# Performance work log

Measured on AMD Instinct MI355X. Metric: run time of the kernel, lower is better.

Reference implementation:

```python
import jax, jax.numpy as jnp
import numpy as np

B, S, H = 2, 2048, 768
NH, HD = 12, 64
I = 1152
EPS = 1e-5
ROPE_BASE = 10000.0
MAX_POS = 8192


def _layernorm(x, w, b):
    mu = jnp.mean(x, axis=-1, keepdims=True)
    var = jnp.mean(jnp.square(x - mu), axis=-1, keepdims=True)
    return (x - mu) / jnp.sqrt(var + EPS) * w + b


def _rope_tables():
    pos = jnp.arange(MAX_POS, dtype=jnp.float32)
    theta = 1.0 / (ROPE_BASE ** (jnp.arange(0, HD, 2, dtype=jnp.float32) / HD))
    ang = pos[:, None] * theta  # [MAX_POS, HD//2]
    return jnp.cos(ang), jnp.sin(ang)


def _apply_rope(x, cos, sin):
    # x: [B, NH, S, HD]; cos/sin: [B, 1, S, HD//2]; interleaved pair rotation
    x2 = x.reshape(*x.shape[:-1], HD // 2, 2)
    x0, x1 = x2[..., 0], x2[..., 1]
    rot = jnp.stack([x0 * cos - x1 * sin, x1 * cos + x0 * sin], axis=-1)
    return rot.reshape(x.shape)


def setup_inputs() -> dict:
    key = jax.random.key(0)
    ks = jax.random.split(key, 8)
    std = 0.02
    return {
        "hidden_states": jax.random.normal(ks[0], (B, S, H), dtype=jnp.float32),
        "attention_mask": jnp.zeros((B, 1, S, S), dtype=jnp.float32),
        "sliding_window_mask": jnp.zeros((B, 1, S, S), dtype=jnp.float32),
        "position_ids": jnp.tile(jnp.arange(S, dtype=jnp.int32)[None, :], (B, 1)),
        "qkv_w": jax.random.normal(ks[1], (3 * H, H), dtype=jnp.float32) * std,
        "o_w": jax.random.normal(ks[2], (H, H), dtype=jnp.float32) * std,
        "attn_norm_w": jnp.ones((H,), dtype=jnp.float32),
        "attn_norm_b": jnp.zeros((H,), dtype=jnp.float32),
        "mlp_norm_w": jnp.ones((H,), dtype=jnp.float32),
        "mlp_norm_b": jnp.zeros((H,), dtype=jnp.float32),
        "wi_w": jax.random.normal(ks[3], (2 * I, H), dtype=jnp.float32) * std,
        "wi_b": jnp.zeros((2 * I,), dtype=jnp.float32),
        "wo_w": jax.random.normal(ks[4], (H, I), dtype=jnp.float32) * std,
        "wo_b": jnp.zeros((H,), dtype=jnp.float32),
    }


def reference(hidden_states, attention_mask, sliding_window_mask, position_ids,
              qkv_w, o_w, attn_norm_w, attn_norm_b, mlp_norm_w, mlp_norm_b,
              wi_w, wi_b, wo_w, wo_b):
    # --- attention block (layer_id != 0 -> pre-LN) ---
    x = _layernorm(hidden_states, attn_norm_w, attn_norm_b)
    qkv = jnp.einsum('bsh,oh->bso', x, qkv_w)          # [B,S,3H] (no bias)
    qkv = qkv.reshape(B, S, 3, NH, HD)
    qkv = jnp.transpose(qkv, (0, 3, 2, 1, 4))          # [B,NH,3,S,HD]
    q, k, v = qkv[:, :, 0], qkv[:, :, 1], qkv[:, :, 2]

    cos_t, sin_t = _rope_tables()
    cos = cos_t[position_ids][:, None]                 # [B,1,S,HD//2]
    sin = sin_t[position_ids][:, None]
    q = _apply_rope(q, cos, sin)
    k = _apply_rope(k, cos, sin)

    scale = HD ** -0.5
    scores = jnp.einsum('bhqd,bhkd->bhqk', q, k) * scale
    scores = scores + attention_mask + sliding_window_mask
    probs = jax.nn.softmax(scores, axis=-1)
    ctx = jnp.einsum('bhqk,bhkd->bhqd', probs, v)      # [B,NH,S,HD]
    ctx = jnp.transpose(ctx, (0, 2, 1, 3)).reshape(B, S, H)
    attn_out = jnp.einsum('bsh,oh->bso', ctx, o_w)
    hidden = hidden_states + attn_out

    # --- GeGLU MLP block ---
    y = _layernorm(hidden, mlp_norm_w, mlp_norm_b)
    h = jax.nn.gelu(jnp.einsum('bsh,oh->bso', y, wi_w) + wi_b, approximate=False)
    gated = h[..., 0::2] * h[..., 1::2]                # strided gelu-gate split
    mlp_out = jnp.einsum('bsi,oi->bso', gated, wo_w) + wo_b
    return hidden + mlp_out
```

## Files before the change

### kernel.cpp

```cpp
#include <hip/hip_runtime.h>
#include <hip/hip_bf16.h>
#include <math.h>

#define B_  2
#define S_  2048
#define H_  768
#define NH_ 12
#define HD_ 64
#define I_  1152
#define LOG2E 1.4426950408889634f
#define SCALE_L2E 0.18033688011112042f

typedef __bf16 bf16;
typedef __bf16 bf16x8 __attribute__((ext_vector_type(8)));
typedef float  f32x4  __attribute__((ext_vector_type(4)));
typedef float  f32x16 __attribute__((ext_vector_type(16)));
typedef float  f32x2  __attribute__((ext_vector_type(2)));
typedef unsigned u32x2 __attribute__((ext_vector_type(2)));
typedef unsigned u32x4 __attribute__((ext_vector_type(4)));

__device__ __forceinline__ void gll16(const void* g, void* l) {
  __builtin_amdgcn_global_load_lds((const __attribute__((address_space(1))) void*)g,
                                   (__attribute__((address_space(3))) void*)l, 16, 0, 0);
}

__device__ __forceinline__ unsigned pack_bf16(float a, float b) {
  union { bf16 e[2]; unsigned u; } r;
  r.e[0] = (bf16)a; r.e[1] = (bf16)b;
  return r.u;
}

__device__ __forceinline__ void plswap(unsigned &a, unsigned &b) {
  asm volatile("v_permlane32_swap_b32 %0, %1" : "+v"(a), "+v"(b));
}
__device__ __forceinline__ float halfmax(float x) {
  unsigned a = __builtin_bit_cast(unsigned, x), b = a;
  plswap(a, b);
  return fmaxf(__builtin_bit_cast(float, a), __builtin_bit_cast(float, b));
}
__device__ __forceinline__ float halfsum(float x) {
  unsigned a = __builtin_bit_cast(unsigned, x), b = a;
  plswap(a, b);
  return __builtin_bit_cast(float, a) + __builtin_bit_cast(float, b);
}

__global__ void cvt_f32_bf16(const float* __restrict__ in, bf16* __restrict__ out, int n4) {
  int i = blockIdx.x * 256 + threadIdx.x;
  if (i >= n4) return;
  float4 v = ((const float4*)in)[i];
  union { bf16 e[4]; uint2 u; } r;
  r.e[0] = (bf16)v.x; r.e[1] = (bf16)v.y; r.e[2] = (bf16)v.z; r.e[3] = (bf16)v.w;
  ((uint2*)out)[i] = r.u;
}

__global__ void build_rope_tbl(f32x2* __restrict__ tbl) {
  int i = blockIdx.x * 256 + threadIdx.x;
  int jp = i & 31, pos = i >> 5;
  float th = exp2f((float)jp * (-13.287712379549449f / 32.f));
  float sn, cs;
  sincosf((float)pos * th, &sn, &cs);
  tbl[i] = (f32x2){cs, sn};
}

__global__ __launch_bounds__(256) void combine_mask2(const float* __restrict__ a,
                                                     const float* __restrict__ b,
                                                     bf16* __restrict__ E,
                                                     unsigned* __restrict__ flags) {
  const int kt = blockIdx.x, qi = blockIdx.y, bb = blockIdx.z, tid = threadIdx.x;
  float sm[8][4];
  bool ok = true;
#pragma unroll
  for (int c = 0; c < 8; ++c) {
    int idx4 = c * 256 + tid;
    int r = idx4 >> 4, col = (idx4 & 15) * 4;
    size_t g = ((size_t)(bb * S_) + qi * 128 + r) * S_ + kt * 64 + col;
    float4 x = *(const float4*)(a + g);
    float4 y = *(const float4*)(b + g);
    sm[c][0] = x.x + y.x; sm[c][1] = x.y + y.y;
    sm[c][2] = x.z + y.z; sm[c][3] = x.w + y.w;
    ok = ok && (sm[c][0] == 0.f) && (sm[c][1] == 0.f) && (sm[c][2] == 0.f) && (sm[c][3] == 0.f);
  }
  __shared__ unsigned sh[4];
  unsigned long long bal = __ballot(ok);
  if ((tid & 63) == 0) sh[tid >> 6] = (bal == ~0ull) ? 1u : 0u;
  __syncthreads();
  unsigned flag = sh[0] & sh[1] & sh[2] & sh[3];
  if (tid == 0) flags[(bb * 16 + qi) * 32 + kt] = flag;
  if (!flag) {
#pragma unroll
    for (int c = 0; c < 8; ++c) {
      int idx4 = c * 256 + tid;
      int r = idx4 >> 4, col = (idx4 & 15) * 4;
      size_t g = ((size_t)(bb * S_) + qi * 128 + r) * S_ + kt * 64 + col;
      union { bf16 e[4]; uint2 u; } w;
      w.e[0] = (bf16)__expf(sm[c][0]); w.e[1] = (bf16)__expf(sm[c][1]);
      w.e[2] = (bf16)__expf(sm[c][2]); w.e[3] = (bf16)__expf(sm[c][3]);
      *(uint2*)(E + g) = w.u;
    }
  }
}

__global__ __launch_bounds__(256) void ln_bf16(const float* __restrict__ in,
                                               const float* __restrict__ w,
                                               const float* __restrict__ bia,
                                               bf16* __restrict__ out) {
  int row = blockIdx.x, tid = threadIdx.x;
  const float* x = in + (size_t)row * H_;
  float v0 = x[tid], v1 = x[tid + 256], v2 = x[tid + 512];
  float s = v0 + v1 + v2;
  float q = v0 * v0 + v1 * v1 + v2 * v2;
  for (int o = 1; o < 64; o <<= 1) { s += __shfl_xor(s, o); q += __shfl_xor(q, o); }
  __shared__ float rs[4], rq[4];
  if ((tid & 63) == 0) { rs[tid >> 6] = s; rq[tid >> 6] = q; }
  __syncthreads();
  s = rs[0] + rs[1] + rs[2] + rs[3];
  q = rq[0] + rq[1] + rq[2] + rq[3];
  float mu = s * (1.f / H_);
  float var = q * (1.f / H_) - mu * mu;
  float rstd = rsqrtf(var + 1e-5f);
  bf16* orow = out + (size_t)row * H_;
  orow[tid]       = (bf16)((v0 - mu) * rstd * w[tid]       + bia[tid]);
  orow[tid + 256] = (bf16)((v1 - mu) * rstd * w[tid + 256] + bia[tid + 256]);
  orow[tid + 512] = (bf16)((v2 - mu) * rstd * w[tid + 512] + bia[tid + 512]);
}

__device__ __forceinline__ void gemm_main_loop(
    int K, const bf16* __restrict__ aSrc0, const bf16* __restrict__ aSrc1,
    const bf16* __restrict__ bSrc0, const bf16* __restrict__ bSrc1,
    bf16* As, bf16* Bs, int tid, int wr, int wc, int l15, int lg,
    f32x4 (&acc)[4][4]) {
  const int NT = K >> 5;
  auto stage = [&](int t, int buf) {
    const int ko = t * 32;
    bf16* ad = As + buf * 4096 + tid * 8;
    bf16* bd = Bs + buf * 4096 + tid * 8;
    gll16(aSrc0 + ko, ad);
    gll16(aSrc1 + ko, ad + 2048);
    gll16(bSrc0 + ko, bd);
    gll16(bSrc1 + ko, bd + 2048);
  };
  stage(0, 0);
  __syncthreads();
  for (int t = 0; t < NT; ++t) {
    const int cur = t & 1;
    if (t + 1 < NT) stage(t + 1, cur ^ 1);
    const bf16* Ab = As + cur * 4096;
    const bf16* Bb = Bs + cur * 4096;
    bf16x8 af[4], bfr[4];
#pragma unroll
    for (int i = 0; i < 4; ++i)
      af[i] = *(const bf16x8*)&Ab[(wr + i * 16 + l15) * 32 + lg * 8];
#pragma unroll
    for (int j = 0; j < 4; ++j)
      bfr[j] = *(const bf16x8*)&Bb[(wc + j * 16 + l15) * 32 + lg * 8];
    __builtin_amdgcn_s_setprio(1);
#pragma unroll
    for (int i = 0; i < 4; ++i)
#pragma unroll
      for (int j = 0; j < 4; ++j)
        acc[i][j] = __builtin_amdgcn_mfma_f32_16x16x32_bf16(af[i], bfr[j], acc[i][j], 0, 0, 0);
    __builtin_amdgcn_s_setprio(0);
    __syncthreads();
  }
}

template<bool BIAS, bool RES>
__global__ __launch_bounds__(256) void gemm128(const bf16* __restrict__ A,
                                               const bf16* __restrict__ W,
                                               float* __restrict__ C,
                                               const float* __restrict__ bias,
                                               const float* __restrict__ res,
                                               int M, int N, int K) {
  __shared__ bf16 As[2 * 128 * 32];
  __shared__ bf16 Bs[2 * 128 * 32];
  const int tid = threadIdx.x, lane = tid & 63, wv = tid >> 6;
  const int bm = blockIdx.y * 128, bn = blockIdx.x * 128;
  const int wr = (wv >> 1) * 64, wc = (wv & 1) * 64;
  const int l15 = lane & 15, lg = lane >> 4;

  f32x4 acc[4][4] = {};
  const int srow = tid >> 2, scc = (tid & 3) * 8;
  gemm_main_loop(K,
      A + (size_t)(bm + srow) * K + scc, A + (size_t)(bm + 64 + srow) * K + scc,
      W + (size_t)(bn + srow) * K + scc, W + (size_t)(bn + 64 + srow) * K + scc,
      As, Bs, tid, wr, wc, l15, lg, acc);

  const int r0 = lg * 4;
#pragma unroll
  for (int i = 0; i < 4; ++i) {
#pragma unroll
    for (int j = 0; j < 4; ++j) {
      int col = bn + wc + j * 16 + l15;
      float bv = BIAS ? bias[col] : 0.f;
#pragma unroll
      for (int r = 0; r < 4; ++r) {
        int row = bm + wr + i * 16 + r0 + r;
        float v = acc[i][j][r] + bv;
        if (RES) v += res[(size_t)row * N + col];
        C[(size_t)row * N + col] = v;
      }
    }
  }
}

__global__ __launch_bounds__(256) void gemm_qkv(const bf16* __restrict__ A,
                                                const bf16* __restrict__ W,
                                                const int* __restrict__ pid,
                                                const f32x2* __restrict__ tbl,
                                                bf16* __restrict__ qb,
                                                bf16* __restrict__ kb,
                                                bf16* __restrict__ vb) {
  __shared__ bf16 As[2 * 128 * 32];
  __shared__ bf16 Bs[2 * 128 * 32];
  const int tid = threadIdx.x, lane = tid & 63, wv = tid >> 6;
  const int bm = blockIdx.y * 128, bn = blockIdx.x * 128;
  const int wr = (wv >> 1) * 64, wc = (wv & 1) * 64;
  const int l15 = lane & 15, lg = lane >> 4;
  const int K = H_;

  f32x4 acc[4][4] = {};
  const int srow = tid >> 2, scc = (tid & 3) * 8;
  gemm_main_loop(K,
      A + (size_t)(bm + srow) * K + scc, A + (size_t)(bm + 64 + srow) * K + scc,
      W + (size_t)(bn + srow) * K + scc, W + (size_t)(bn + 64 + srow) * K + scc,
      As, Bs, tid, wr, wc, l15, lg, acc);

  const int r0 = lg * 4;
  const int sect = bn / H_;
  const int hcb = (bn % H_) + wc;
  bf16* dst0 = sect == 0 ? qb : (sect == 1 ? kb : vb);
#pragma unroll
  for (int i = 0; i < 4; ++i) {
#pragma unroll
    for (int r = 0; r < 4; ++r) {
      const int row = bm + wr + i * 16 + r0 + r;
      const int b = row >> 11, s = row & 2047;
      const int pos = (sect < 2) ? pid[row] : 0;
#pragma unroll
      for (int j = 0; j < 4; ++j) {
        const int hc = hcb + j * 16 + l15;
        const int h = hc >> 6, d = hc & 63;
        float x = acc[i][j][r];
        float v;
        if (sect < 2) {
          f32x2 cs = tbl[pos * 32 + (d >> 1)];
          float xp = __shfl_xor(x, 1);
          v = (d & 1) ? fmaf(x, cs.x, xp * cs.y) : fmaf(x, cs.x, -xp * cs.y);
        } else {
          v = x;
        }
        dst0[((size_t)(b * NH_ + h) * S_ + s) * HD_ + d] = (bf16)v;
      }
    }
  }
}

__global__ __launch_bounds__(256) void gemm_wi(const bf16* __restrict__ A,
                                               const bf16* __restrict__ W,
                                               const float* __restrict__ bias,
                                               bf16* __restrict__ g) {
  __shared__ bf16 As[2 * 128 * 32];
  __shared__ bf16 Bs[2 * 128 * 32];
  const int tid = threadIdx.x, lane = tid & 63, wv = tid >> 6;
  const int bm = blockIdx.y * 128, bn = blockIdx.x * 128;
  const int wr = (wv >> 1) * 64, wc = (wv & 1) * 64;
  const int l15 = lane & 15, lg = lane >> 4;
  const int K = H_;

  f32x4 acc[4][4] = {};
  const int srow = tid >> 2, scc = (tid & 3) * 8;
  gemm_main_loop(K,
      A + (size_t)(bm + srow) * K + scc, A + (size_t)(bm + 64 + srow) * K + scc,
      W + (size_t)(bn + srow) * K + scc, W + (size_t)(bn + 64 + srow) * K + scc,
      As, Bs, tid, wr, wc, l15, lg, acc);

  const int r0 = lg * 4;
#pragma unroll
  for (int j = 0; j < 4; ++j) {
    const int col = bn + wc + j * 16 + l15;
    const float bv = bias[col];
#pragma unroll
    for (int i = 0; i < 4; ++i) {
#pragma unroll
      for (int r = 0; r < 4; ++r) {
        const int row = bm + wr + i * 16 + r0 + r;
        float x = acc[i][j][r] + bv;
        float gx = 0.5f * x * (1.f + erff(x * 0.70710678118654752f));
        float gp = __shfl_xor(gx, 1);
        if (!(l15 & 1))
          g[(size_t)row * I_ + (col >> 1)] = (bf16)(gx * gp);
      }
    }
  }
}

__global__ __launch_bounds__(512, 4) void attn8(
    const bf16* __restrict__ Q, const bf16* __restrict__ Kg, const bf16* __restrict__ Vg,
    const bf16* __restrict__ Eg, const unsigned* __restrict__ flags, bf16* __restrict__ ctx) {
  __shared__ bf16 Kt[2][2][64 * 64];
  __shared__ bf16 Vt[2][2][64 * 64];
  const int tid = threadIdx.x, lane = tid & 63, wv = tid >> 6;
  const int wq = wv & 3, ks = wv >> 2;
  const int qi = blockIdx.x, h = blockIdx.y, b = blockIdx.z;
  const int l31 = lane & 31, hi = lane >> 5, b4 = (lane >> 4) & 1;
  const size_t headbase = (size_t)(b * NH_ + h) * S_ * HD_;
  const bf16* kbase = Kg + headbase;
  const bf16* vbase = Vg + headbase;
  const unsigned* fptr = flags + (b * 16 + qi) * 32;
  const int kswz = (l31 & 7) << 4;
  const int qrow = qi * 128 + wq * 32 + l31;
  const bf16* Erow = Eg + (size_t)b * S_ * S_ + (size_t)qrow * S_;

  bf16x8 qf[4];
  {
    const bf16* qp = Q + headbase + (size_t)qrow * HD_;
#pragma unroll
    for (int kc = 0; kc < 4; ++kc)
      qf[kc] = *(const bf16x8*)(qp + kc * 16 + hi * 8);
  }

  auto stageK = [&](int t, int bs, int par) {
    int kr = tid >> 3, sl = tid & 7;
    gll16(kbase + (size_t)t * 64 * HD_ + kr * HD_ + (sl ^ (kr & 7)) * 8, &Kt[bs][par][tid * 8]);
  };
  auto stageV = [&](int t, int bs, int par) {
    int p = tid >> 7, kr = (tid & 127) >> 1, hf = tid & 1;
    gll16(vbase + (size_t)t * 64 * HD_ + kr * HD_ + (p >> 1) * 32 + (p & 1) * 16 + hf * 8,
          &Vt[bs][par][tid * 8]);
  };

  float m = -1e30f, l = 0.f;
  f32x16 oa[2] = {};

  stageK(0, 0, 0); stageV(0, 0, 0);
  stageK(1, 0, 1); stageV(1, 0, 1);
  unsigned fl = fptr[ks];
  __syncthreads();

  for (int r = 0; r < 16; ++r) {
    const int cur = r & 1;
    const int kt = 2 * r + ks;
    unsigned flN = 1;
    if (r < 15) {
      flN = fptr[kt + 2];
      stageK(2 * r + 2, cur ^ 1, 0); stageV(2 * r + 2, cur ^ 1, 0);
      stageK(2 * r + 3, cur ^ 1, 1); stageV(2 * r + 3, cur ^ 1, 1);
    }

    f32x16 sv[2];
    __builtin_amdgcn_s_setprio(1);
#pragma unroll
    for (int kb = 0; kb < 2; ++kb) {
      f32x16 s = {};
#pragma unroll
      for (int kc = 0; kc < 4; ++kc) {
        const bf16x8 kf = *(const bf16x8*)((const char*)&Kt[cur][ks][0] +
            ((kb * 32 + l31) * 128 + ((kc * 32 + hi * 16) ^ kswz)));
        s = __builtin_amdgcn_mfma_f32_32x32x16_bf16(kf, qf[kc], s, 0, 0, 0);
      }
      sv[kb] = s;
    }
    __builtin_amdgcn_s_setprio(0);

    float p0 = fmaxf(sv[0][0], sv[1][0]), p1 = fmaxf(sv[0][1], sv[1][1]);
    float p2 = fmaxf(sv[0][2], sv[1][2]), p3 = fmaxf(sv[0][3], sv[1][3]);
#pragma unroll
    for (int r2 = 4; r2 < 16; r2 += 4) {
      p0 = fmaxf(p0, fmaxf(sv[0][r2],     sv[1][r2]));
      p1 = fmaxf(p1, fmaxf(sv[0][r2 + 1], sv[1][r2 + 1]));
      p2 = fmaxf(p2, fmaxf(sv[0][r2 + 2], sv[1][r2 + 2]));
      p3 = fmaxf(p3, fmaxf(sv[0][r2 + 3], sv[1][r2 + 3]));
    }
    float pmS = halfmax(fmaxf(fmaxf(p0, p1), fmaxf(p2, p3))) * SCALE_L2E;
    if (__any(pmS - m > 8.f)) {
      float mn = fmaxf(m, pmS);
      float alpha = exp2f(m - mn);
      m = mn;
      l *= alpha;
#pragma unroll
      for (int db = 0; db < 2; ++db)
#pragma unroll
        for (int r2 = 0; r2 < 16; ++r2) oa[db][r2] *= alpha;
    }
#pragma unroll
    for (int kb = 0; kb < 2; ++kb)
#pragma unroll
      for (int r2 = 0; r2 < 16; ++r2)
        sv[kb][r2] = exp2f(fmaf(sv[kb][r2], SCALE_L2E, -m));
    if (!fl) {
#pragma unroll
      for (int kb = 0; kb < 2; ++kb)
#pragma unroll
        for (int rq = 0; rq < 4; ++rq) {
          union { bf16 e[4]; u32x2 u; } eu;
          eu.u = *(const u32x2*)(Erow + (size_t)kt * 64 + kb * 32 + rq * 8 + hi * 4);
#pragma unroll
          for (int j = 0; j < 4; ++j)
            sv[kb][rq * 4 + j] *= (float)eu.e[j];
        }
    }
    float s0 = sv[0][0] + sv[1][0], s1 = sv[0][1] + sv[1][1];
    float s2 = sv[0][2] + sv[1][2], s3 = sv[0][3] + sv[1][3];
#pragma unroll
    for (int r2 = 4; r2 < 16; r2 += 4) {
      s0 += sv[0][r2]     + sv[1][r2];
      s1 += sv[0][r2 + 1] + sv[1][r2 + 1];
      s2 += sv[0][r2 + 2] + sv[1][r2 + 2];
      s3 += sv[0][r2 + 3] + sv[1][r2 + 3];
    }
    l += halfsum((s0 + s1) + (s2 + s3));

    unsigned pk[2][4][2];
#pragma unroll
    for (int kb = 0; kb < 2; ++kb)
#pragma unroll
      for (int rq = 0; rq < 4; ++rq)
#pragma unroll
        for (int dd = 0; dd < 2; ++dd)
          pk[kb][rq][dd] = pack_bf16(sv[kb][rq * 4 + dd * 2], sv[kb][rq * 4 + dd * 2 + 1]);
    unsigned pa[4][4];
#pragma unroll
    for (int kc = 0; kc < 4; ++kc) {
      const int kb = kc >> 1, rb = (kc & 1) * 2;
#pragma unroll
      for (int dd = 0; dd < 2; ++dd) {
        unsigned A = pk[kb][rb][dd], Bv = pk[kb][rb + 1][dd];
        plswap(A, Bv);
        pa[kc][dd] = A; pa[kc][2 + dd] = Bv;
      }
    }

    const unsigned vlds = (unsigned)(size_t)&Vt[cur][ks][0] + b4 * 1920;
#pragma unroll
    for (int db = 0; db < 2; ++db) {
      u32x2 tr[4][2];
#pragma unroll
      for (int kc = 0; kc < 4; ++kc)
#pragma unroll
        for (int rd = 0; rd < 2; ++rd) {
          unsigned ad = vlds + (db * 4096 + kc * 512 + rd * 128);
          asm volatile("ds_read_b64_tr_b16 %0, %1 offset:0" : "=v"(tr[kc][rd]) : "v"(ad));
        }
      asm volatile("s_waitcnt lgkmcnt(0)" ::: "memory");
      __builtin_amdgcn_sched_barrier(0);
      __builtin_amdgcn_s_setprio(1);
#pragma unroll
      for (int kc = 0; kc < 4; ++kc) {
        union { u32x4 u; bf16x8 v; } vfu, pau;
        vfu.u = (u32x4){tr[kc][0][0], tr[kc][0][1], tr[kc][1][0], tr[kc][1][1]};
        pau.u = (u32x4){pa[kc][0], pa[kc][1], pa[kc][2], pa[kc][3]};
        oa[db] = __builtin_amdgcn_mfma_f32_32x32x16_bf16(vfu.v, pau.v, oa[db], 0, 0, 0);
      }
      __builtin_amdgcn_s_setprio(0);
    }
    __syncthreads();
    fl = flN;
  }

  float* KO = (float*)&Kt[0][0][0];
  float* ML = (float*)&Vt[1][0][0];
  if (ks == 1) {
#pragma unroll
    for (int db = 0; db < 2; ++db)
#pragma unroll
      for (int rq = 0; rq < 4; ++rq) {
        int q4 = (db * 4 + rq) ^ (l31 & 7);
        *(f32x4*)&KO[wq * 2048 + l31 * 64 + hi * 32 + q4 * 4] =
            (f32x4){oa[db][rq * 4], oa[db][rq * 4 + 1], oa[db][rq * 4 + 2], oa[db][rq * 4 + 3]};
      }
    if (hi == 0) { ML[wq * 64 + l31 * 2] = m; ML[wq * 64 + l31 * 2 + 1] = l; }
  }
  __syncthreads();
  if (ks == 0) {
    float m1 = ML[wq * 64 + l31 * 2], l1 = ML[wq * 64 + l31 * 2 + 1];
    float ms = fmaxf(m, m1);
    float a0 = exp2f(m - ms), a1 = exp2f(m1 - ms);
    float inv = 1.f / (l * a0 + l1 * a1);
    a0 *= inv; a1 *= inv;
    char* TR = (char*)&Vt[0][0][0];
#pragma unroll
    for (int db = 0; db < 2; ++db)
#pragma unroll
      for (int rq = 0; rq < 4; ++rq) {
        int q4 = (db * 4 + rq) ^ (l31 & 7);
        f32x4 o1 = *(const f32x4*)&KO[wq * 2048 + l31 * 64 + hi * 32 + q4 * 4];
        float f0 = oa[db][rq * 4 + 0] * a0 + o1[0] * a1;
        float f1 = oa[db][rq * 4 + 1] * a0 + o1[1] * a1;
        float f2 = oa[db][rq * 4 + 2] * a0 + o1[2] * a1;
        float f3 = oa[db][rq * 4 + 3] * a0 + o1[3] * a1;
        u32x2 w = (u32x2){pack_bf16(f0, f1), pack_bf16(f2, f3)};
        *(u32x2*)(TR + wq * 4096 + l31 * 128 + ((db * 64 + rq * 16 + hi * 8) ^ kswz)) = w;
      }
  }
  __syncthreads();
#pragma unroll
  for (int c = 0; c < 2; ++c) {
    int ch = c * 512 + tid, q = ch >> 3, sl = ch & 7;
    u32x4 vv = *(const u32x4*)((const char*)&Vt[0][0][0] +
        ((q >> 5) * 4096 + (q & 31) * 128 + ((sl ^ (q & 7)) * 16)));
    *(u32x4*)(ctx + ((size_t)(b * S_) + qi * 128 + q) * H_ + h * HD_ + sl * 8) = vv;
  }
}

extern "C" void kernel_launch(void* const* d_in, const int* in_sizes, int n_in,
                              void* d_out, int out_size, void* d_ws, size_t ws_size,
                              hipStream_t stream) {
  const float* hs   = (const float*)d_in[0];
  const float* am   = (const float*)d_in[1];
  const float* swm  = (const float*)d_in[2];
  const int*   pid  = (const int*)d_in[3];
  const float* qkvw = (const float*)d_in[4];
  const float* ow   = (const float*)d_in[5];
  const float* anw  = (const float*)d_in[6];
  const float* anb  = (const float*)d_in[7];
  const float* mnw  = (const float*)d_in[8];
  const float* mnb  = (const float*)d_in[9];
  const float* wiw  = (const float*)d_in[10];
  const float* wib  = (const float*)d_in[11];
  const float* wow  = (const float*)d_in[12];
  const float* wob  = (const float*)d_in[13];
  float* out = (float*)d_out;

  char* ws = (char*)d_ws;
  size_t off = 0;
  auto alloc = [&](size_t bytes) { void* p = ws + off; off += (bytes + 255) & ~255ull; return p; };

  bf16* wqkv_b = (bf16*)alloc((size_t)3 * H_ * H_ * 2);
  bf16* wo_b   = (bf16*)alloc((size_t)H_ * H_ * 2);
  bf16* wwi_b  = (bf16*)alloc((size_t)2 * I_ * H_ * 2);
  bf16* wwo_b  = (bf16*)alloc((size_t)H_ * I_ * 2);
  bf16* xln    = (bf16*)alloc((size_t)B_ * S_ * H_ * 2);
  bf16* qb     = (bf16*)alloc((size_t)B_ * NH_ * S_ * HD_ * 2);
  bf16* kb     = (bf16*)alloc((size_t)B_ * NH_ * S_ * HD_ * 2);
  bf16* vb     = (bf16*)alloc((size_t)B_ * NH_ * S_ * HD_ * 2);
  bf16* Eg     = (bf16*)alloc((size_t)B_ * S_ * S_ * 2);
  unsigned* flg= (unsigned*)alloc((size_t)B_ * 16 * 32 * 4);
  bf16* ctx    = (bf16*)alloc((size_t)B_ * S_ * H_ * 2);
  float* hid2  = (float*)alloc((size_t)B_ * S_ * H_ * 4);
  bf16* gated  = (bf16*)alloc((size_t)B_ * S_ * I_ * 2);
  f32x2* tbl   = (f32x2*)alloc((size_t)8192 * 32 * 8);
  (void)ws_size; (void)n_in; (void)in_sizes; (void)out_size;

  const int rows = B_ * S_;

  cvt_f32_bf16<<<(3 * H_ * H_ / 4 + 255) / 256, 256, 0, stream>>>(qkvw, wqkv_b, 3 * H_ * H_ / 4);
  cvt_f32_bf16<<<(H_ * H_ / 4 + 255) / 256, 256, 0, stream>>>(ow, wo_b, H_ * H_ / 4);
  cvt_f32_bf16<<<(2 * I_ * H_ / 4 + 255) / 256, 256, 0, stream>>>(wiw, wwi_b, 2 * I_ * H_ / 4);
  cvt_f32_bf16<<<(H_ * I_ / 4 + 255) / 256, 256, 0, stream>>>(wow, wwo_b, H_ * I_ / 4);
  build_rope_tbl<<<8192 * 32 / 256, 256, 0, stream>>>(tbl);
  combine_mask2<<<dim3(32, 16, B_), 256, 0, stream>>>(am, swm, Eg, flg);

  ln_bf16<<<rows, 256, 0, stream>>>(hs, anw, anb, xln);
  gemm_qkv<<<dim3(3 * H_ / 128, rows / 128), 256, 0, stream>>>(
      xln, wqkv_b, pid, tbl, qb, kb, vb);
  attn8<<<dim3(S_ / 128, NH_, B_), 512, 0, stream>>>(qb, kb, vb, Eg, flg, ctx);
  gemm128<false, true><<<dim3(H_ / 128, rows / 128), 256, 0, stream>>>(
      ctx, wo_b, hid2, nullptr, hs, rows, H_, H_);
  ln_bf16<<<rows, 256, 0, stream>>>(hid2, mnw, mnb, xln);
  gemm_wi<<<dim3(2 * I_ / 128, rows / 128), 256, 0, stream>>>(xln, wwi_b, wib, gated);
  gemm128<true, true><<<dim3(H_ / 128, rows / 128), 256, 0, stream>>>(
      gated, wwo_b, out, wob, hid2, rows, H_, I_);
}
```

Measured before the change: 233.1 us.

## Drop LDS double buffering and use 64-row tiles for output GEMMs

Replaces the double-buffered, priority-boosted GEMM main loop with a single-buffered loop that syncs before and after each K-tile load. It adds a 64x128 tile GEMM for the o-proj and wo GEMMs, doubling their block count from 192 to 384 so more CUs are used. The single buffer halves LDS use but serialises global loads against MFMA work, which may stall the QKV and wi GEMMs. The extra blocks also reload the weight tiles more often.

New measurement: 240.1 us. 1.03x slower.

```diff
diff --git a/kernel.cpp b/kernel.cpp
--- a/kernel.cpp
+++ b/kernel.cpp
@@ -124,70 +124,76 @@
   orow[tid + 512] = (bf16)((v2 - mu) * rstd * w[tid + 512] + bia[tid + 512]);
 }
 
-__device__ __forceinline__ void gemm_main_loop(
+__device__ __forceinline__ void gemm_loop128(
     int K, const bf16* __restrict__ aSrc0, const bf16* __restrict__ aSrc1,
     const bf16* __restrict__ bSrc0, const bf16* __restrict__ bSrc1,
     bf16* As, bf16* Bs, int tid, int wr, int wc, int l15, int lg,
     f32x4 (&acc)[4][4]) {
-  const int NT = K >> 5;
-  auto stage = [&](int t, int buf) {
-    const int ko = t * 32;
-    bf16* ad = As + buf * 4096 + tid * 8;
-    bf16* bd = Bs + buf * 4096 + tid * 8;
-    gll16(aSrc0 + ko, ad);
-    gll16(aSrc1 + ko, ad + 2048);
-    gll16(bSrc0 + ko, bd);
-    gll16(bSrc1 + ko, bd + 2048);
-  };
-  stage(0, 0);
-  __syncthreads();
-  for (int t = 0; t < NT; ++t) {
-    const int cur = t & 1;
-    if (t + 1 < NT) stage(t + 1, cur ^ 1);
-    const bf16* Ab = As + cur * 4096;
-    const bf16* Bb = Bs + cur * 4096;
+  for (int k0 = 0; k0 < K; k0 += 32) {
+    __syncthreads();
+    gll16(aSrc0 + k0, As + tid * 8);
+    gll16(aSrc1 + k0, As + 2048 + tid * 8);
+    gll16(bSrc0 + k0, Bs + tid * 8);
+    gll16(bSrc1 + k0, Bs + 2048 + tid * 8);
+    __syncthreads();
     bf16x8 af[4], bfr[4];
 #pragma unroll
     for (int i = 0; i < 4; ++i)
-      af[i] = *(const bf16x8*)&Ab[(wr + i * 16 + l15) * 32 + lg * 8];
+      af[i] = *(const bf16x8*)&As[(wr + i * 16 + l15) * 32 + lg * 8];
 #pragma unroll
     for (int j = 0; j < 4; ++j)
-      bfr[j] = *(const bf16x8*)&Bb[(wc + j * 16 + l15) * 32 + lg * 8];
-    __builtin_amdgcn_s_setprio(1);
+      bfr[j] = *(const bf16x8*)&Bs[(wc + j * 16 + l15) * 32 + lg * 8];
 #pragma unroll
     for (int i = 0; i < 4; ++i)
 #pragma unroll
       for (int j = 0; j < 4; ++j)
         acc[i][j] = __builtin_amdgcn_mfma_f32_16x16x32_bf16(af[i], bfr[j], acc[i][j], 0, 0, 0);
-    __builtin_amdgcn_s_setprio(0);
+  }
+}
+
+template<bool BIAS, bool RES>
+__global__ __launch_bounds__(256) void gemm64(const bf16* __restrict__ A,
+                                              const bf16* __restrict__ W,
+                                              float* __restrict__ C,
+                                              const float* __restrict__ bias,
+                                              const float* __restrict__ res,
+                                              int M, int N, int K) {
+  __shared__ bf16 As[64 * 32];
+  __shared__ bf16 Bs[128 * 32];
+  const int tid = threadIdx.x, lane = tid & 63, wv = tid >> 6;
+  const int bm = blockIdx.y * 64, bn = blockIdx.x * 128;
+  const int wr = (wv >> 1) * 32, wc = (wv & 1) * 64;
+  const int l15 = lane & 15, lg = lane >> 4;
+
+  f32x4 acc[2][4] = {};
+  const int srow = tid >> 2, scc = (tid & 3) * 8;
+  const bf16* aSrc0 = A + (size_t)(bm + srow) * K + scc;
+  const bf16* bSrc0 = W + (size_t)(bn + srow) * K + scc;
+  const bf16* bSrc1 = W + (size_t)(bn + 64 + srow) * K + scc;
+
+  for (int k0 = 0; k0 < K; k0 += 32) {
     __syncthreads();
-  }
-}
-
-template<bool BIAS, bool RES>
-__global__ __launch_bounds__(256) void gemm128(const bf16* __restrict__ A,
-                                               const bf16* __restrict__ W,
-                                               float* __restrict__ C,
-                                               const float* __restrict__ bias,
-                                               const float* __restrict__ res,
-                                               int M, int N, int K) {
-  __shared__ bf16 As[2 * 128 * 32];
-  __shared__ bf16 Bs[2 * 128 * 32];
-  const int tid = threadIdx.x, lane = tid & 63, wv = tid >> 6;
-  const int bm = blockIdx.y * 128, bn = blockIdx.x * 128;
-  const int wr = (wv >> 1) * 64, wc = (wv & 1) * 64;
-  const int l15 = lane & 15, lg = lane >> 4;
-
-  f32x4 acc[4][4] = {};
-  const int srow = tid >> 2, scc = (tid & 3) * 8;
-  gemm_main_loop(K,
-      A + (size_t)(bm + srow) * K + scc, A + (size_t)(bm + 64 + srow) * K + scc,
-      W + (size_t)(bn + srow) * K + scc, W + (size_t)(bn + 64 + srow) * K + scc,
-      As, Bs, tid, wr, wc, l15, lg, acc);
+    gll16(aSrc0 + k0, As + tid * 8);
+    gll16(bSrc0 + k0, Bs + tid * 8);
+    gll16(bSrc1 + k0, Bs + 2048 + tid * 8);
+    __syncthreads();
+    bf16x8 af[2], bfr[4];
+#pragma unroll
+    for (int i = 0; i < 2; ++i)
+      af[i] = *(const bf16x8*)&As[(wr + i * 16 + l15) * 32 + lg * 8];
+#pragma unroll
+    for (int j = 0; j < 4; ++j)
+      bfr[j] = *(const bf16x8*)&Bs[(wc + j * 16 + l15) * 32 + lg * 8];
+#pragma unroll
+    for (int i = 0; i < 2; ++i)
+#pragma unroll
+      for (int j = 0; j < 4; ++j)
+        acc[i][j] = __builtin_amdgcn_mfma_f32_16x16x32_bf16(af[i], bfr[j], acc[i][j], 0, 0, 0);
+  }
 
   const int r0 = lg * 4;
 #pragma unroll
-  for (int i = 0; i < 4; ++i) {
+  for (int i = 0; i < 2; ++i) {
 #pragma unroll
     for (int j = 0; j < 4; ++j) {
       int col = bn + wc + j * 16 + l15;
@@ -210,8 +216,8 @@
                                                 bf16* __restrict__ qb,
                                                 bf16* __restrict__ kb,
                                                 bf16* __restrict__ vb) {
-  __shared__ bf16 As[2 * 128 * 32];
-  __shared__ bf16 Bs[2 * 128 * 32];
+  __shared__ bf16 As[128 * 32];
+  __shared__ bf16 Bs[128 * 32];
   const int tid = threadIdx.x, lane = tid & 63, wv = tid >> 6;
   const int bm = blockIdx.y * 128, bn = blockIdx.x * 128;
   const int wr = (wv >> 1) * 64, wc = (wv & 1) * 64;
@@ -220,7 +226,7 @@
 
   f32x4 acc[4][4] = {};
   const int srow = tid >> 2, scc = (tid & 3) * 8;
-  gemm_main_loop(K,
+  gemm_loop128(K,
       A + (size_t)(bm + srow) * K + scc, A + (size_t)(bm + 64 + srow) * K + scc,
       W + (size_t)(bn + srow) * K + scc, W + (size_t)(bn + 64 + srow) * K + scc,
       As, Bs, tid, wr, wc, l15, lg, acc);
@@ -259,8 +265,8 @@
                                                const bf16* __restrict__ W,
                                                const float* __restrict__ bias,
                                                bf16* __restrict__ g) {
-  __shared__ bf16 As[2 * 128 * 32];
-  __shared__ bf16 Bs[2 * 128 * 32];
+  __shared__ bf16 As[128 * 32];
+  __shared__ bf16 Bs[128 * 32];
   const int tid = threadIdx.x, lane = tid & 63, wv = tid >> 6;
   const int bm = blockIdx.y * 128, bn = blockIdx.x * 128;
   const int wr = (wv >> 1) * 64, wc = (wv & 1) * 64;
@@ -269,7 +275,7 @@
 
   f32x4 acc[4][4] = {};
   const int srow = tid >> 2, scc = (tid & 3) * 8;
-  gemm_main_loop(K,
+  gemm_loop128(K,
       A + (size_t)(bm + srow) * K + scc, A + (size_t)(bm + 64 + srow) * K + scc,
       W + (size_t)(bn + srow) * K + scc, W + (size_t)(bn + 64 + srow) * K + scc,
       As, Bs, tid, wr, wc, l15, lg, acc);
@@ -554,10 +560,10 @@
   gemm_qkv<<<dim3(3 * H_ / 128, rows / 128), 256, 0, stream>>>(
       xln, wqkv_b, pid, tbl, qb, kb, vb);
   attn8<<<dim3(S_ / 128, NH_, B_), 512, 0, stream>>>(qb, kb, vb, Eg, flg, ctx);
-  gemm128<false, true><<<dim3(H_ / 128, rows / 128), 256, 0, stream>>>(
+  gemm64<false, true><<<dim3(H_ / 128, rows / 64), 256, 0, stream>>>(
       ctx, wo_b, hid2, nullptr, hs, rows, H_, H_);
   ln_bf16<<<rows, 256, 0, stream>>>(hid2, mnw, mnb, xln);
   gemm_wi<<<dim3(2 * I_ / 128, rows / 128), 256, 0, stream>>>(xln, wwi_b, wib, gated);
-  gemm128<true, true><<<dim3(H_ / 128, rows / 128), 256, 0, stream>>>(
+  gemm64<true, true><<<dim3(H_ / 128, rows / 64), 256, 0, stream>>>(
       gated, wwo_b, out, wob, hid2, rows, H_, I_);
 }
```

## Shrink attention blocks to 64 query rows and keep K in registers

Applied to the files above, without the earlier changes.

The attention kernel now uses 256-thread blocks covering 64 query rows instead of 512-thread blocks covering 128, which doubles the grid so it spreads more evenly across CUs. K tiles are no longer staged through LDS. Each wave loads them straight from global memory into double-buffered registers, and only V stays in LDS. The epilogue reuses the V buffers for the cross-split merge and the output transpose. In exchange, the two query waves that share a key split each fetch the same K data, and register pressure rises, which could limit occupancy.

Result: slower. 267.5 us (+14.8%).

```diff
diff --git a/kernel.cpp b/kernel.cpp
--- a/kernel.cpp
+++ b/kernel.cpp
@@ -294,21 +294,20 @@
   }
 }
 
-__global__ __launch_bounds__(512, 4) void attn8(
+__global__ __launch_bounds__(256, 3) void attn4(
     const bf16* __restrict__ Q, const bf16* __restrict__ Kg, const bf16* __restrict__ Vg,
     const bf16* __restrict__ Eg, const unsigned* __restrict__ flags, bf16* __restrict__ ctx) {
-  __shared__ bf16 Kt[2][2][64 * 64];
   __shared__ bf16 Vt[2][2][64 * 64];
   const int tid = threadIdx.x, lane = tid & 63, wv = tid >> 6;
-  const int wq = wv & 3, ks = wv >> 2;
+  const int wq = wv & 1, ks = wv >> 1;
   const int qi = blockIdx.x, h = blockIdx.y, b = blockIdx.z;
   const int l31 = lane & 31, hi = lane >> 5, b4 = (lane >> 4) & 1;
   const size_t headbase = (size_t)(b * NH_ + h) * S_ * HD_;
   const bf16* kbase = Kg + headbase;
   const bf16* vbase = Vg + headbase;
-  const unsigned* fptr = flags + (b * 16 + qi) * 32;
+  const unsigned* fptr = flags + (b * 16 + (qi >> 1)) * 32;
   const int kswz = (l31 & 7) << 4;
-  const int qrow = qi * 128 + wq * 32 + l31;
+  const int qrow = qi * 64 + wq * 32 + l31;
   const bf16* Erow = Eg + (size_t)b * S_ * S_ + (size_t)qrow * S_;
 
   bf16x8 qf[4];
@@ -319,32 +318,41 @@
       qf[kc] = *(const bf16x8*)(qp + kc * 16 + hi * 8);
   }
 
-  auto stageK = [&](int t, int bs, int par) {
-    int kr = tid >> 3, sl = tid & 7;
-    gll16(kbase + (size_t)t * 64 * HD_ + kr * HD_ + (sl ^ (kr & 7)) * 8, &Kt[bs][par][tid * 8]);
+  auto stageV = [&](int t, int bs, int par) {
+#pragma unroll
+    for (int c = 0; c < 2; ++c) {
+      int ch = c * 256 + tid;
+      int p = ch >> 7, kr = (ch & 127) >> 1, hf = ch & 1;
+      gll16(vbase + (size_t)t * 64 * HD_ + kr * HD_ + (p >> 1) * 32 + (p & 1) * 16 + hf * 8,
+            &Vt[bs][par][ch * 8]);
+    }
   };
-  auto stageV = [&](int t, int bs, int par) {
-    int p = tid >> 7, kr = (tid & 127) >> 1, hf = tid & 1;
-    gll16(vbase + (size_t)t * 64 * HD_ + kr * HD_ + (p >> 1) * 32 + (p & 1) * 16 + hf * 8,
-          &Vt[bs][par][tid * 8]);
+  auto loadK = [&](int t, bf16x8 (&dst)[2][4]) {
+#pragma unroll
+    for (int kb = 0; kb < 2; ++kb)
+#pragma unroll
+      for (int kc = 0; kc < 4; ++kc)
+        dst[kb][kc] = *(const bf16x8*)(kbase +
+            (size_t)(t * 64 + kb * 32 + l31) * HD_ + kc * 16 + hi * 8);
   };
 
   float m = -1e30f, l = 0.f;
   f32x16 oa[2] = {};
-
-  stageK(0, 0, 0); stageV(0, 0, 0);
-  stageK(1, 0, 1); stageV(1, 0, 1);
+  bf16x8 kfA[2][4], kfB[2][4];
+
+  stageV(0, 0, 0); stageV(1, 0, 1);
+  loadK(ks, kfA);
   unsigned fl = fptr[ks];
   __syncthreads();
 
-  for (int r = 0; r < 16; ++r) {
-    const int cur = r & 1;
-    const int kt = 2 * r + ks;
+  auto step = [&](int R, int cur, bf16x8 (&KC)[2][4], bf16x8 (&KN)[2][4]) {
+    const int kt = 2 * R + ks;
     unsigned flN = 1;
-    if (r < 15) {
+    if (R < 15) {
       flN = fptr[kt + 2];
-      stageK(2 * r + 2, cur ^ 1, 0); stageV(2 * r + 2, cur ^ 1, 0);
-      stageK(2 * r + 3, cur ^ 1, 1); stageV(2 * r + 3, cur ^ 1, 1);
+      stageV(2 * R + 2, cur ^ 1, 0);
+      stageV(2 * R + 3, cur ^ 1, 1);
+      loadK(kt + 2, KN);
     }
 
     f32x16 sv[2];
@@ -353,11 +361,8 @@
     for (int kb = 0; kb < 2; ++kb) {
       f32x16 s = {};
 #pragma unroll
-      for (int kc = 0; kc < 4; ++kc) {
-        const bf16x8 kf = *(const bf16x8*)((const char*)&Kt[cur][ks][0] +
-            ((kb * 32 + l31) * 128 + ((kc * 32 + hi * 16) ^ kswz)));
-        s = __builtin_amdgcn_mfma_f32_32x32x16_bf16(kf, qf[kc], s, 0, 0, 0);
-      }
+      for (int kc = 0; kc < 4; ++kc)
+        s = __builtin_amdgcn_mfma_f32_32x32x16_bf16(KC[kb][kc], qf[kc], s, 0, 0, 0);
       sv[kb] = s;
     }
     __builtin_amdgcn_s_setprio(0);
@@ -441,7 +446,7 @@
           unsigned ad = vlds + (db * 4096 + kc * 512 + rd * 128);
           asm volatile("ds_read_b64_tr_b16 %0, %1 offset:0" : "=v"(tr[kc][rd]) : "v"(ad));
         }
-      asm volatile("s_waitcnt lgkmcnt(0)" ::: "memory");
+    asm volatile("s_waitcnt lgkmcnt(0)" ::: "memory");
       __builtin_amdgcn_sched_barrier(0);
       __builtin_amdgcn_s_setprio(1);
 #pragma unroll
@@ -455,10 +460,16 @@
     }
     __syncthreads();
     fl = flN;
-  }
-
-  float* KO = (float*)&Kt[0][0][0];
+  };
+
+  for (int rr = 0; rr < 8; ++rr) {
+    step(2 * rr,     0, kfA, kfB);
+    step(2 * rr + 1, 1, kfB, kfA);
+  }
+
+  float* KO = (float*)&Vt[0][0][0];
   float* ML = (float*)&Vt[1][0][0];
+  char*  TR = (char*)&Vt[1][0][0] + 512;
   if (ks == 1) {
 #pragma unroll
     for (int db = 0; db < 2; ++db)
@@ -477,7 +488,6 @@
     float a0 = exp2f(m - ms), a1 = exp2f(m1 - ms);
     float inv = 1.f / (l * a0 + l1 * a1);
     a0 *= inv; a1 *= inv;
-    char* TR = (char*)&Vt[0][0][0];
 #pragma unroll
     for (int db = 0; db < 2; ++db)
 #pragma unroll
@@ -495,10 +505,9 @@
   __syncthreads();
 #pragma unroll
   for (int c = 0; c < 2; ++c) {
-    int ch = c * 512 + tid, q = ch >> 3, sl = ch & 7;
-    u32x4 vv = *(const u32x4*)((const char*)&Vt[0][0][0] +
-        ((q >> 5) * 4096 + (q & 31) * 128 + ((sl ^ (q & 7)) * 16)));
-    *(u32x4*)(ctx + ((size_t)(b * S_) + qi * 128 + q) * H_ + h * HD_ + sl * 8) = vv;
+    int ch = c * 256 + tid, q = ch >> 3, sl = ch & 7;
+    u32x4 vv = *(const u32x4*)(TR + ((q >> 5) * 4096 + (q & 31) * 128 + ((sl ^ (q & 7)) * 16)));
+    *(u32x4*)(ctx + ((size_t)(b * S_) + qi * 64 + q) * H_ + h * HD_ + sl * 8) = vv;
   }
 }
 
@@ -553,7 +562,7 @@
   ln_bf16<<<rows, 256, 0, stream>>>(hs, anw, anb, xln);
   gemm_qkv<<<dim3(3 * H_ / 128, rows / 128), 256, 0, stream>>>(
       xln, wqkv_b, pid, tbl, qb, kb, vb);
-  attn8<<<dim3(S_ / 128, NH_, B_), 512, 0, stream>>>(qb, kb, vb, Eg, flg, ctx);
+  attn4<<<dim3(S_ / 64, NH_, B_), 256, 0, stream>>>(qb, kb, vb, Eg, flg, ctx);
   gemm128<false, true><<<dim3(H_ / 128, rows / 128), 256, 0, stream>>>(
       ctx, wo_b, hid2, nullptr, hs, rows, H_, H_);
   ln_bf16<<<rows, 256, 0, stream>>>(hid2, mnw, mnb, xln);
```
